# Performance work log

Hardware: AMD Instinct MI355X
Metric: run time of the kernel (lower is better)

The kernel has to match this reference:

```python
import jax, jax.numpy as jnp
import numpy as np

HIDDEN = 1024
HEADS = 16
HEAD_DIM = HIDDEN // HEADS
SCALE = float(np.sqrt(HEAD_DIM))


def setup_inputs() -> dict:
    key = jax.random.key(0)
    ks = jax.random.split(key, 5)
    x = jax.random.normal(ks[0], (2, 2048, HIDDEN), dtype=jnp.float32)
    # qkv_proj: Linear(hidden, 3*hidden); torch stores weight as [out, in]
    w_qkv = jax.random.normal(ks[1], (3 * HIDDEN, HIDDEN), dtype=jnp.float32) / np.sqrt(HIDDEN)
    b_qkv = jax.random.normal(ks[2], (3 * HIDDEN,), dtype=jnp.float32) * 0.02
    w_out = jax.random.normal(ks[3], (HIDDEN, HIDDEN), dtype=jnp.float32) / np.sqrt(HIDDEN)
    b_out = jax.random.normal(ks[4], (HIDDEN,), dtype=jnp.float32) * 0.02
    return {"x": x, "w_qkv": w_qkv, "b_qkv": b_qkv, "w_out": w_out, "b_out": b_out}


def reference(x, w_qkv, b_qkv, w_out, b_out):
    B, S, H = x.shape
    # fused QKV projection -> [B, S, 3, heads, head_dim]
    qkv = (jnp.einsum('bsh,oh->bso', x, w_qkv) + b_qkv).reshape(B, S, 3, HEADS, HEAD_DIM)
    q, k, v = qkv[:, :, 0], qkv[:, :, 1], qkv[:, :, 2]
    scores = jnp.einsum('bqhd,bkhd->bhqk', q, k) / SCALE
    attn = jax.nn.softmax(scores, axis=-1)  # dropout p=0.0 (eval)
    ctx = jnp.einsum('bhqk,bkhd->bqhd', attn, v).reshape(B, S, H)
    return jnp.einsum('bsh,oh->bso', ctx, w_out) + b_out
```

## Files before the change

### kernel.cpp

```cpp
#include <hip/hip_runtime.h>
#include <math.h>

#define BATCH 2
#define SEQ   2048
#define HIDDEN 1024
#define HEADS 16
#define HD    64
#define QSCALE 0.18033688011112042f

typedef __attribute__((ext_vector_type(8)))  short short8;
typedef __attribute__((ext_vector_type(16))) float f32x16;

__device__ __forceinline__ unsigned short f2bf(float f) {
    unsigned int u = __builtin_bit_cast(unsigned int, f);
    u = (u + 0x7FFFu + ((u >> 16) & 1u)) >> 16;
    return (unsigned short)u;
}
__device__ __forceinline__ float bf2f(unsigned short h) {
    unsigned int u = ((unsigned int)h) << 16;
    return __builtin_bit_cast(float, u);
}
__device__ __forceinline__ unsigned int cvt_pk_bf16(float lo, float hi) {
    unsigned int r;
    asm("v_cvt_pk_bf16_f32 %0, %1, %2" : "=v"(r) : "v"(lo), "v"(hi));
    return r;
}
__device__ __forceinline__ void gl16(const void* g, void* l) {
    __builtin_amdgcn_global_load_lds(
        (const __attribute__((address_space(1))) void*)g,
        (__attribute__((address_space(3))) void*)l,
        16, 0, 0);
}
#define WAIT_VM(N) asm volatile("s_waitcnt vmcnt(" #N ")" ::: "memory")
#define BARRIER()  do { __builtin_amdgcn_s_barrier(); __builtin_amdgcn_sched_barrier(0); } while (0)

__global__ __launch_bounds__(256)
void conv_hi(const float* __restrict__ src, unsigned short* __restrict__ hi)
{
    int idx = blockIdx.x * 256 + threadIdx.x;
    float4 v = ((const float4*)src)[idx];
    ushort4 h4;
    h4.x = f2bf(v.x); h4.y = f2bf(v.y); h4.z = f2bf(v.z); h4.w = f2bf(v.w);
    ((ushort4*)hi)[idx] = h4;
}

__device__ __forceinline__ void gemm_core1(
    const char* Ah, const char* Bh,
    int m0, int n0, char* smem, f32x16 acc[2][2])
{
    const int t    = threadIdx.x;
    const int lane = t & 63;
    const int w    = t >> 6;
    const int wm   = w >> 1, wn = w & 1;
    const int l31  = lane & 31, hh = lane >> 5;

    auto stage = [&](int buf, int kt) {
        #pragma unroll
        for (int i = 0; i < 2; ++i) {
            int r  = i * 64 + (t >> 2);
            int cs = (t & 3) ^ ((r >> 1) & 3);
            gl16(Ah + ((size_t)(m0 + r) * 1024 + kt * 32 + cs * 8) * 2,
                 smem + buf * 16384 + i * 4096 + w * 1024);
            gl16(Bh + ((size_t)(n0 + r) * 1024 + kt * 32 + cs * 8) * 2,
                 smem + buf * 16384 + 8192 + i * 4096 + w * 1024);
        }
    };

    stage(0, 0);
    __syncthreads();

    for (int kt = 0; kt < 32; ++kt) {
        if (kt + 1 < 32) stage((kt & 1) ^ 1, kt + 1);
        const char* Ab = smem + (kt & 1) * 16384;
        const char* Bb = Ab + 8192;
        #pragma unroll
        for (int ks = 0; ks < 2; ++ks) {
            short8 ah[2], bh[2];
            #pragma unroll
            for (int mt = 0; mt < 2; ++mt) {
                int R  = wm * 64 + mt * 32 + l31;
                int ch = ((ks * 2 + hh) ^ ((R >> 1) & 3)) * 16;
                ah[mt] = *(const short8*)(Ab + R * 64 + ch);
            }
            #pragma unroll
            for (int nt = 0; nt < 2; ++nt) {
                int R  = wn * 64 + nt * 32 + l31;
                int ch = ((ks * 2 + hh) ^ ((R >> 1) & 3)) * 16;
                bh[nt] = *(const short8*)(Bb + R * 64 + ch);
            }
            #pragma unroll
            for (int mt = 0; mt < 2; ++mt)
                #pragma unroll
                for (int nt = 0; nt < 2; ++nt)
                    acc[mt][nt] = __builtin_amdgcn_mfma_f32_32x32x16_bf16(ah[mt], bh[nt], acc[mt][nt], 0, 0, 0);
        }
        __syncthreads();
    }
}

__global__ __launch_bounds__(256, 3)
void qkv_gemm(const unsigned short* __restrict__ xh,
              const unsigned short* __restrict__ wh,
              const float* __restrict__ bias,
              unsigned short* __restrict__ qB, unsigned short* __restrict__ kB,
              unsigned short* __restrict__ vtB)
{
    __shared__ __align__(16) char smem[34816];
    f32x16 acc[2][2] = {{{}, {}}, {{}, {}}};
    const int m0 = blockIdx.x * 128, n0 = blockIdx.y * 128;
    gemm_core1((const char*)xh, (const char*)wh, m0, n0, smem, acc);

    const int t    = threadIdx.x;
    const int lane = t & 63;
    const int w    = t >> 6;
    const int wm   = w >> 1, wn = w & 1;
    const int l31  = lane & 31, hh = lane >> 5;

    const int which = n0 >> 10;
    const float scl = (which == 0) ? QSCALE : 1.0f;

    #pragma unroll
    for (int mt = 0; mt < 2; ++mt)
        #pragma unroll
        for (int nt = 0; nt < 2; ++nt) {
            int nl = wn * 64 + nt * 32 + l31;
            float bb = bias[n0 + nl];
            #pragma unroll
            for (int r = 0; r < 16; ++r) {
                int ml = wm * 64 + mt * 32 + (r & 3) + 8 * (r >> 2) + 4 * hh;
                float val = (acc[mt][nt][r] + bb) * scl;
                *(unsigned short*)(smem + ml * 272 + nl * 2) = f2bf(val);
            }
        }
    __syncthreads();

    const int hbase = (n0 & 1023) >> 6;
    const int b     = m0 >> 11;
    const int s0    = m0 & 2047;

    if (which < 2) {
        unsigned short* pp = which ? kB : qB;
        const int nc   = t & 31;
        const int head = hbase + (nc >> 4);
        const int d0   = (nc & 15) * 4;
        #pragma unroll
        for (int it = 0; it < 16; ++it) {
            int m = it * 8 + (t >> 5);
            ushort4 h4 = *(const ushort4*)(smem + m * 272 + nc * 8);
            size_t idx = (((size_t)(b * HEADS + head)) * SEQ + s0 + m) * HD + d0;
            *(ushort4*)&pp[idx] = h4;
        }
    } else {
        const int nl   = t & 127;
        const int head = hbase + (nl >> 6);
        const int d    = nl & 63;
        #pragma unroll
        for (int it = 0; it < 16; ++it) {
            int mq = it * 2 + (t >> 7);
            ushort4 h4;
            h4.x = *(const unsigned short*)(smem + (mq * 4 + 0) * 272 + nl * 2);
            h4.y = *(const unsigned short*)(smem + (mq * 4 + 1) * 272 + nl * 2);
            h4.z = *(const unsigned short*)(smem + (mq * 4 + 2) * 272 + nl * 2);
            h4.w = *(const unsigned short*)(smem + (mq * 4 + 3) * 272 + nl * 2);
            size_t idx = (((size_t)(b * HEADS + head)) * HD + d) * SEQ + s0 + mq * 4;
            *(ushort4*)&vtB[idx] = h4;
        }
    }
}

__global__ __launch_bounds__(256, 3)
void out_gemm(const unsigned short* __restrict__ cth,
              const unsigned short* __restrict__ bh_,
              const float* __restrict__ bias, float* __restrict__ out)
{
    __shared__ __align__(16) char smem[32768];
    f32x16 acc[2][2] = {{{}, {}}, {{}, {}}};
    const int m0 = blockIdx.x * 128, n0 = blockIdx.y * 128;
    gemm_core1((const char*)cth, (const char*)bh_, m0, n0, smem, acc);

    const int t    = threadIdx.x;
    const int lane = t & 63;
    const int w    = t >> 6;
    const int wm   = w >> 1, wn = w & 1;
    const int l31  = lane & 31, hh = lane >> 5;

    #pragma unroll
    for (int mt = 0; mt < 2; ++mt)
        #pragma unroll
        for (int nt = 0; nt < 2; ++nt) {
            int n = n0 + wn * 64 + nt * 32 + l31;
            float bb = bias[n];
            #pragma unroll
            for (int r = 0; r < 16; ++r) {
                int m = m0 + wm * 64 + mt * 32 + (r & 3) + 8 * (r >> 2) + 4 * hh;
                out[(size_t)m * 1024 + n] = acc[mt][nt][r] + bb;
            }
        }
}

#define NPAIR (SEQ / 64)

__global__ __launch_bounds__(256, 2)
void attn_mfma(const unsigned short* __restrict__ qB, const unsigned short* __restrict__ kB,
               const unsigned short* __restrict__ vtB, unsigned short* __restrict__ ctxb)
{
    __shared__ __align__(16) char smem[65536];
    const int t    = threadIdx.x;
    const int lane = t & 63;
    const int wq   = t >> 6;
    const int l31  = lane & 31;
    const int hh   = lane >> 5;

    const int bid = blockIdx.x;
    const int xcd = bid & 7, j = bid >> 3;
    const int qt  = j & 15;
    const int bhg = xcd + 8 * (j >> 4);
    const int q0  = qt * 128;
    const size_t bh = (size_t)bhg;

    const char* qP = (const char*)(qB + bh * SEQ * HD);
    const char* kP = (const char*)(kB + bh * SEQ * HD);
    const char* vP = (const char*)(vtB + bh * SEQ * HD);

    const int wbase = wq * 1024;

    {
        int rr = t >> 3, cc = t & 7;
        #pragma unroll
        for (int i = 0; i < 4; ++i) {
            int row = i * 32 + rr;
            int ch  = cc ^ (row & 7);
            gl16(qP + (size_t)(q0 + row) * 128 + ch * 16, smem + i * 4096 + wbase);
        }
    }
    auto stagePair = [&](int p) {
        int base = ((p + 1) & 3) * 16384;
        int rr = t >> 3;
        int ch = (t & 7) ^ (rr & 7);
        gl16(kP + (size_t)(p * 64 + rr) * 128 + ch * 16,      smem + base +     0 + wbase);
        gl16(kP + (size_t)(p * 64 + 32 + rr) * 128 + ch * 16, smem + base +  4096 + wbase);
        int rr2 = t >> 2;
        int s4  = (rr2 & 3) ^ ((rr2 >> 2) & 3);
        int ch2 = (t & 3) ^ s4;
        gl16(vP + (size_t)rr2 * (SEQ * 2) + p * 128 +      ch2 * 16, smem + base +  8192 + wbase);
        gl16(vP + (size_t)rr2 * (SEQ * 2) + p * 128 + 64 + ch2 * 16, smem + base + 12288 + wbase);
    };
    stagePair(0);
    stagePair(1);
    WAIT_VM(8);
    BARRIER();

    short8 qf[4];
    {
        int qrow = 32 * wq + l31;
        #pragma unroll
        for (int ks = 0; ks < 4; ++ks) {
            int ch = ((2 * ks + hh) ^ (qrow & 7)) * 16;
            qf[ks] = *(const short8*)(smem + qrow * 128 + ch);
        }
    }
    asm volatile("s_waitcnt lgkmcnt(0)" ::: "memory");
    __builtin_amdgcn_sched_barrier(0);

    f32x16 acc0 = {}, acc1 = {};
    float lsum = 0.0f;

    for (int i = 0; i < NPAIR; ++i) {
        if (i + 2 < NPAIR) { stagePair(i + 2); WAIT_VM(8); }
        else if (i + 1 < NPAIR) { WAIT_VM(4); }
        else { WAIT_VM(0); }
        BARRIER();

        const char* Pb = smem + ((i + 1) & 3) * 16384;

        f32x16 sa = {}, sb = {};
        __builtin_amdgcn_s_setprio(1);
        #pragma unroll
        for (int ks = 0; ks < 4; ++ks) {
            int ch = ((2 * ks + hh) ^ (l31 & 7)) * 16;
            short8 ka = *(const short8*)(Pb +        l31 * 128 + ch);
            short8 kb = *(const short8*)(Pb + 4096 + l31 * 128 + ch);
            sa = __builtin_amdgcn_mfma_f32_32x32x16_bf16(ka, qf[ks], sa, 0, 0, 0);
            sb = __builtin_amdgcn_mfma_f32_32x32x16_bf16(kb, qf[ks], sb, 0, 0, 0);
        }
        __builtin_amdgcn_s_setprio(0);

        unsigned int pa_[8], pb_[8];
        float ps0 = 0.f, ps1 = 0.f, ps2 = 0.f, ps3 = 0.f;
        #pragma unroll
        for (int w = 0; w < 8; ++w) {
            float e0 = __builtin_amdgcn_exp2f(sa[2 * w]);
            float e1 = __builtin_amdgcn_exp2f(sa[2 * w + 1]);
            ps0 += e0; ps1 += e1;
            pa_[w] = cvt_pk_bf16(e0, e1);
            float f0 = __builtin_amdgcn_exp2f(sb[2 * w]);
            float f1 = __builtin_amdgcn_exp2f(sb[2 * w + 1]);
            ps2 += f0; ps3 += f1;
            pb_[w] = cvt_pk_bf16(f0, f1);
        }
        lsum += (ps0 + ps1) + (ps2 + ps3);

        const char* Va = Pb + 8192;
        const char* Vb = Pb + 12288;
        __builtin_amdgcn_s_setprio(1);
        #pragma unroll
        for (int ks = 0; ks < 2; ++ks) {
            unsigned int a0 = pa_[4*ks],     a2 = pa_[4*ks + 2];
            unsigned int a1 = pa_[4*ks + 1], a3 = pa_[4*ks + 3];
            asm volatile("v_permlane32_swap_b32 %0, %1" : "+v"(a0), "+v"(a2));
            asm volatile("v_permlane32_swap_b32 %0, %1" : "+v"(a1), "+v"(a3));
            unsigned int b0 = pb_[4*ks],     b2 = pb_[4*ks + 2];
            unsigned int b1 = pb_[4*ks + 1], b3 = pb_[4*ks + 3];
            asm volatile("v_permlane32_swap_b32 %0, %1" : "+v"(b0), "+v"(b2));
            asm volatile("v_permlane32_swap_b32 %0, %1" : "+v"(b1), "+v"(b3));
            short8 pA = __builtin_bit_cast(short8, make_uint4(a0, a1, a2, a3));
            short8 pB = __builtin_bit_cast(short8, make_uint4(b0, b1, b2, b3));
            #pragma unroll
            for (int mt = 0; mt < 2; ++mt) {
                int rrow = 32 * mt + l31;
                int s4   = (rrow & 3) ^ ((rrow >> 2) & 3);
                int ch   = ((2 * ks + hh) ^ s4) * 16;
                short8 va = *(const short8*)(Va + rrow * 64 + ch);
                short8 vb = *(const short8*)(Vb + rrow * 64 + ch);
                if (mt == 0) {
                    acc0 = __builtin_amdgcn_mfma_f32_32x32x16_bf16(va, pA, acc0, 0, 0, 0);
                    acc0 = __builtin_amdgcn_mfma_f32_32x32x16_bf16(vb, pB, acc0, 0, 0, 0);
                } else {
                    acc1 = __builtin_amdgcn_mfma_f32_32x32x16_bf16(va, pA, acc1, 0, 0, 0);
                    acc1 = __builtin_amdgcn_mfma_f32_32x32x16_bf16(vb, pB, acc1, 0, 0, 0);
                }
            }
        }
        __builtin_amdgcn_s_setprio(0);
    }

    lsum += __shfl_xor(lsum, 32, 64);
    __syncthreads();
    float inv = 1.0f / lsum;
    {
        int q = 32 * wq + l31;
        #pragma unroll
        for (int mt = 0; mt < 2; ++mt) {
            #pragma unroll
            for (int m2 = 0; m2 < 4; ++m2) {
                ushort4 h4;
                if (mt == 0) {
                    h4.x = f2bf(acc0[4*m2+0] * inv); h4.y = f2bf(acc0[4*m2+1] * inv);
                    h4.z = f2bf(acc0[4*m2+2] * inv); h4.w = f2bf(acc0[4*m2+3] * inv);
                } else {
                    h4.x = f2bf(acc1[4*m2+0] * inv); h4.y = f2bf(acc1[4*m2+1] * inv);
                    h4.z = f2bf(acc1[4*m2+2] * inv); h4.w = f2bf(acc1[4*m2+3] * inv);
                }
                int d0 = 4 * hh + 8 * m2 + 32 * mt;
                int c  = (d0 >> 3) ^ (q & 7);
                *(ushort4*)(smem + q * 128 + c * 16 + (d0 & 7) * 2) = h4;
            }
        }
    }
    __syncthreads();
    {
        #pragma unroll
        for (int it = 0; it < 4; ++it) {
            int slot = it * 256 + t;
            int row  = slot >> 3;
            int p    = slot & 7;
            uint4 v4 = *(const uint4*)(smem + row * 128 + ((p ^ (row & 7)) * 16));
            *(uint4*)&ctxb[((size_t)(bhg >> 4) * SEQ + q0 + row) * HIDDEN
                           + (bhg & 15) * HD + p * 8] = v4;
        }
    }
}

extern "C" void kernel_launch(void* const* d_in, const int* in_sizes, int n_in,
                              void* d_out, int out_size, void* d_ws, size_t ws_size,
                              hipStream_t stream)
{
    const float* x     = (const float*)d_in[0];
    const float* w_qkv = (const float*)d_in[1];
    const float* b_qkv = (const float*)d_in[2];
    const float* w_out = (const float*)d_in[3];
    const float* b_out = (const float*)d_in[4];
    float* out = (float*)d_out;

    const size_t PH = (size_t)BATCH * HEADS * SEQ * HD;
    unsigned short* ws = (unsigned short*)d_ws;
    unsigned short* qB  = ws;
    unsigned short* kB  = ws + PH;
    unsigned short* vtB = ws + 2 * PH;
    unsigned short* wqh = ws + 3 * PH;
    unsigned short* woh = wqh + 3 * PH / 4;
    unsigned short* cth = woh + PH / 4;
    unsigned short* xh  = (unsigned short*)d_out;

    conv_hi<<<4096, 256, 0, stream>>>(x, xh);
    conv_hi<<<3072, 256, 0, stream>>>(w_qkv, wqh);
    conv_hi<<<1024, 256, 0, stream>>>(w_out, woh);
    qkv_gemm<<<dim3(32, 24), 256, 0, stream>>>(xh, wqh, b_qkv, qB, kB, vtB);
    attn_mfma<<<512, 256, 0, stream>>>(qB, kB, vtB, cth);
    out_gemm<<<dim3(32, 8), 256, 0, stream>>>(cth, woh, b_out, out);
}
```

Measured before the change: 116.0 us.

## Split attention over two key halves with fp32 partials and a combine kernel

The attention kernel now processes only half of the key/value sequence per block, doubling the grid to 1024 blocks. Each block writes unnormalised fp32 accumulators and row sums to scratch buffers (reusing the output buffer and the converted QKV-weight buffer). A new combine kernel adds the two halves, normalises, and writes the bf16 context. Shared memory drops to triple buffering so three blocks can be resident per CU, aiming for better occupancy and CU fill. The cost is an extra launch and a large fp32 round trip through global memory.

```diff
diff --git a/kernel.cpp b/kernel.cpp
--- a/kernel.cpp
+++ b/kernel.cpp
@@ -198,24 +198,28 @@
         }
 }
 
-#define NPAIR (SEQ / 64)
-
-__global__ __launch_bounds__(256, 2)
+#define NPH 16
+
+__global__ __launch_bounds__(256, 3)
 void attn_mfma(const unsigned short* __restrict__ qB, const unsigned short* __restrict__ kB,
-               const unsigned short* __restrict__ vtB, unsigned short* __restrict__ ctxb)
-{
-    __shared__ __align__(16) char smem[65536];
+               const unsigned short* __restrict__ vtB,
+               float* __restrict__ pacc0, float* __restrict__ pacc1,
+               float* __restrict__ plsum)
+{
+    __shared__ __align__(16) char smem[49152];
     const int t    = threadIdx.x;
     const int lane = t & 63;
     const int wq   = t >> 6;
     const int l31  = lane & 31;
     const int hh   = lane >> 5;
 
-    const int bid = blockIdx.x;
-    const int xcd = bid & 7, j = bid >> 3;
-    const int qt  = j & 15;
-    const int bhg = xcd + 8 * (j >> 4);
-    const int q0  = qt * 128;
+    const int bid  = blockIdx.x;
+    const int xcd  = bid & 7;
+    const int r    = bid >> 3;
+    const int qt   = r & 15;
+    const int bhg  = xcd + 8 * ((r >> 4) & 3);
+    const int half = r >> 6;
+    const int q0   = qt * 128;
     const size_t bh = (size_t)bhg;
 
     const char* qP = (const char*)(qB + bh * SEQ * HD);
@@ -230,24 +234,25 @@
         for (int i = 0; i < 4; ++i) {
             int row = i * 32 + rr;
             int ch  = cc ^ (row & 7);
-            gl16(qP + (size_t)(q0 + row) * 128 + ch * 16, smem + i * 4096 + wbase);
-        }
-    }
-    auto stagePair = [&](int p) {
-        int base = ((p + 1) & 3) * 16384;
+            gl16(qP + (size_t)(q0 + row) * 128 + ch * 16,
+                 smem + 16384 + i * 4096 + wbase);
+        }
+    }
+    auto stagePair = [&](int b, int g) {
+        int base = b * 16384;
         int rr = t >> 3;
         int ch = (t & 7) ^ (rr & 7);
-        gl16(kP + (size_t)(p * 64 + rr) * 128 + ch * 16,      smem + base +     0 + wbase);
-        gl16(kP + (size_t)(p * 64 + 32 + rr) * 128 + ch * 16, smem + base +  4096 + wbase);
+        gl16(kP + (size_t)(g * 64 + rr) * 128 + ch * 16,      smem + base +     0 + wbase);
+        gl16(kP + (size_t)(g * 64 + 32 + rr) * 128 + ch * 16, smem + base +  4096 + wbase);
         int rr2 = t >> 2;
         int s4  = (rr2 & 3) ^ ((rr2 >> 2) & 3);
         int ch2 = (t & 3) ^ s4;
-        gl16(vP + (size_t)rr2 * (SEQ * 2) + p * 128 +      ch2 * 16, smem + base +  8192 + wbase);
-        gl16(vP + (size_t)rr2 * (SEQ * 2) + p * 128 + 64 + ch2 * 16, smem + base + 12288 + wbase);
+        gl16(vP + (size_t)rr2 * (SEQ * 2) + g * 128 +      ch2 * 16, smem + base +  8192 + wbase);
+        gl16(vP + (size_t)rr2 * (SEQ * 2) + g * 128 + 64 + ch2 * 16, smem + base + 12288 + wbase);
     };
-    stagePair(0);
-    stagePair(1);
-    WAIT_VM(8);
+    const int g0 = half * NPH;
+    stagePair(0, g0);
+    WAIT_VM(4);
     BARRIER();
 
     short8 qf[4];
@@ -256,22 +261,27 @@
         #pragma unroll
         for (int ks = 0; ks < 4; ++ks) {
             int ch = ((2 * ks + hh) ^ (qrow & 7)) * 16;
-            qf[ks] = *(const short8*)(smem + qrow * 128 + ch);
+            qf[ks] = *(const short8*)(smem + 16384 + qrow * 128 + ch);
         }
     }
     asm volatile("s_waitcnt lgkmcnt(0)" ::: "memory");
     __builtin_amdgcn_sched_barrier(0);
+    BARRIER();
 
     f32x16 acc0 = {}, acc1 = {};
     float lsum = 0.0f;
 
-    for (int i = 0; i < NPAIR; ++i) {
-        if (i + 2 < NPAIR) { stagePair(i + 2); WAIT_VM(8); }
-        else if (i + 1 < NPAIR) { WAIT_VM(4); }
-        else { WAIT_VM(0); }
+    for (int i = 0; i < NPH; ++i) {
+        if (i + 1 < NPH) {
+            int nx = i + 1;
+            stagePair(nx - (nx / 3) * 3, g0 + nx);
+            WAIT_VM(4);
+        } else {
+            WAIT_VM(0);
+        }
         BARRIER();
 
-        const char* Pb = smem + ((i + 1) & 3) * 16384;
+        const char* Pb = smem + (i - (i / 3) * 3) * 16384;
 
         f32x16 sa = {}, sb = {};
         __builtin_amdgcn_s_setprio(1);
@@ -335,39 +345,63 @@
     }
 
     lsum += __shfl_xor(lsum, 32, 64);
+    const int tile = bhg * 16 + qt;
+    float* dst = (half ? pacc1 : pacc0) + (size_t)tile * 8192 + t * 32;
+    #pragma unroll
+    for (int m2 = 0; m2 < 4; ++m2) {
+        *(float4*)(dst + m2 * 4)      = make_float4(acc0[4*m2+0], acc0[4*m2+1], acc0[4*m2+2], acc0[4*m2+3]);
+        *(float4*)(dst + 16 + m2 * 4) = make_float4(acc1[4*m2+0], acc1[4*m2+1], acc1[4*m2+2], acc1[4*m2+3]);
+    }
+    if (hh == 0)
+        plsum[(size_t)(half * 512 + tile) * 128 + 32 * wq + l31] = lsum;
+}
+
+__global__ __launch_bounds__(256, 2)
+void attn_combine(const float* __restrict__ pacc0, const float* __restrict__ pacc1,
+                  const float* __restrict__ plsum, unsigned short* __restrict__ ctxb)
+{
+    __shared__ __align__(16) char smem[16384];
+    const int t    = threadIdx.x;
+    const int lane = t & 63;
+    const int wq   = t >> 6;
+    const int l31  = lane & 31;
+    const int hh   = lane >> 5;
+    const int tile = blockIdx.x;
+    const int bhg  = tile >> 4;
+    const int q0   = (tile & 15) * 128;
+    const int q    = 32 * wq + l31;
+
+    const float* A = pacc0 + (size_t)tile * 8192 + t * 32;
+    const float* B = pacc1 + (size_t)tile * 8192 + t * 32;
+    float l0 = plsum[(size_t)tile * 128 + q];
+    float l1 = plsum[(size_t)(512 + tile) * 128 + q];
+    float inv = 1.0f / (l0 + l1);
+
+    #pragma unroll
+    for (int mt = 0; mt < 2; ++mt)
+        #pragma unroll
+        for (int m2 = 0; m2 < 4; ++m2) {
+            int off = mt * 16 + m2 * 4;
+            float4 a = *(const float4*)(A + off);
+            float4 b = *(const float4*)(B + off);
+            ushort4 h4;
+            h4.x = f2bf((a.x + b.x) * inv);
+            h4.y = f2bf((a.y + b.y) * inv);
+            h4.z = f2bf((a.z + b.z) * inv);
+            h4.w = f2bf((a.w + b.w) * inv);
+            int d0 = 4 * hh + 8 * m2 + 32 * mt;
+            int c  = (d0 >> 3) ^ (q & 7);
+            *(ushort4*)(smem + q * 128 + c * 16 + (d0 & 7) * 2) = h4;
+        }
     __syncthreads();
-    float inv = 1.0f / lsum;
-    {
-        int q = 32 * wq + l31;
-        #pragma unroll
-        for (int mt = 0; mt < 2; ++mt) {
-            #pragma unroll
-            for (int m2 = 0; m2 < 4; ++m2) {
-                ushort4 h4;
-                if (mt == 0) {
-                    h4.x = f2bf(acc0[4*m2+0] * inv); h4.y = f2bf(acc0[4*m2+1] * inv);
-                    h4.z = f2bf(acc0[4*m2+2] * inv); h4.w = f2bf(acc0[4*m2+3] * inv);
-                } else {
-                    h4.x = f2bf(acc1[4*m2+0] * inv); h4.y = f2bf(acc1[4*m2+1] * inv);
-                    h4.z = f2bf(acc1[4*m2+2] * inv); h4.w = f2bf(acc1[4*m2+3] * inv);
-                }
-                int d0 = 4 * hh + 8 * m2 + 32 * mt;
-                int c  = (d0 >> 3) ^ (q & 7);
-                *(ushort4*)(smem + q * 128 + c * 16 + (d0 & 7) * 2) = h4;
-            }
-        }
-    }
-    __syncthreads();
-    {
-        #pragma unroll
-        for (int it = 0; it < 4; ++it) {
-            int slot = it * 256 + t;
-            int row  = slot >> 3;
-            int p    = slot & 7;
-            uint4 v4 = *(const uint4*)(smem + row * 128 + ((p ^ (row & 7)) * 16));
-            *(uint4*)&ctxb[((size_t)(bhg >> 4) * SEQ + q0 + row) * HIDDEN
-                           + (bhg & 15) * HD + p * 8] = v4;
-        }
+    #pragma unroll
+    for (int it = 0; it < 4; ++it) {
+        int slot = it * 256 + t;
+        int row  = slot >> 3;
+        int p    = slot & 7;
+        uint4 v4 = *(const uint4*)(smem + row * 128 + ((p ^ (row & 7)) * 16));
+        *(uint4*)&ctxb[((size_t)(bhg >> 4) * SEQ + q0 + row) * HIDDEN
+                       + (bhg & 15) * HD + p * 8] = v4;
     }
 }
 
@@ -390,12 +424,16 @@
     unsigned short* wqh = ws + 3 * PH;
     unsigned short* woh = wqh + 3 * PH / 4;
     unsigned short* cth = woh + PH / 4;
-    unsigned short* xh  = (unsigned short*)d_out;
+    float* pacc1 = (float*)(ws + 6 * PH);
+    float* plsum = (float*)wqh;
+    unsigned short* xh = (unsigned short*)d_out;
+    float* pacc0 = (float*)d_out;
 
     conv_hi<<<4096, 256, 0, stream>>>(x, xh);
     conv_hi<<<3072, 256, 0, stream>>>(w_qkv, wqh);
     conv_hi<<<1024, 256, 0, stream>>>(w_out, woh);
     qkv_gemm<<<dim3(32, 24), 256, 0, stream>>>(xh, wqh, b_qkv, qB, kB, vtB);
-    attn_mfma<<<512, 256, 0, stream>>>(qB, kB, vtB, cth);
+    attn_mfma<<<1024, 256, 0, stream>>>(qB, kB, vtB, pacc0, pacc1, plsum);
+    attn_combine<<<512, 256, 0, stream>>>(pacc0, pacc1, plsum, cth);
     out_gemm<<<dim3(32, 8), 256, 0, stream>>>(cth, woh, b_out, out);
 }
```

New measurement: 129.9 us. 12.0% more time.
